# Performance work log

Hardware: AMD Instinct MI355X
Metric: run time of the kernel (lower is better)

The kernel has to match this reference:

```python
import jax, jax.numpy as jnp
import numpy as np

N_NODES = 100000
N_EDGES = 3200000
IN_FEAT = 512
HIDDEN = 64
N_GRAPHS = 2048


def setup_inputs() -> dict:
    key = jax.random.key(0)
    ks = jax.random.split(key, 8)
    x = jax.random.normal(ks[0], (N_NODES, IN_FEAT), dtype=jnp.float32)
    edge_index = jax.random.randint(ks[1], (2, N_EDGES), 0, N_NODES, dtype=jnp.int64)
    batch = jnp.sort(jax.random.randint(ks[2], (N_NODES,), 0, N_GRAPHS, dtype=jnp.int64))
    W1 = jax.random.normal(ks[3], (IN_FEAT, HIDDEN), dtype=jnp.float32) * (1.0 / np.sqrt(IN_FEAT))
    b1 = jnp.zeros((HIDDEN,), dtype=jnp.float32)
    W2 = jax.random.normal(ks[4], (HIDDEN, HIDDEN), dtype=jnp.float32) * (1.0 / np.sqrt(HIDDEN))
    b2 = jnp.zeros((HIDDEN,), dtype=jnp.float32)
    fc_w = jax.random.normal(ks[5], (HIDDEN, 1), dtype=jnp.float32) * (1.0 / np.sqrt(HIDDEN))
    fc_b = jnp.zeros((1,), dtype=jnp.float32)
    return {"x": x, "edge_index": edge_index, "batch": batch, "num_graphs": N_GRAPHS,
            "W1": W1, "b1": b1, "W2": W2, "b2": b2, "fc_w": fc_w, "fc_b": fc_b}


def _gcn_conv(x, src, dst, n_nodes, W, b):
    # PyG GCNConv: h = X W; out = D^{-1/2}(A+I)D^{-1/2} h + b  (self-loops already in src/dst)
    h = x @ W  # [N, out]
    ones = jnp.ones_like(src, dtype=h.dtype)
    deg = jax.ops.segment_sum(ones, dst, num_segments=n_nodes)  # in-degree incl. self-loop
    dinv = jnp.where(deg > 0, jax.lax.rsqrt(deg), 0.0)
    norm = dinv[src] * dinv[dst]  # [E+N]
    msgs = h[src] * norm[:, None]  # gather + scale
    out = jax.ops.segment_sum(msgs, dst, num_segments=n_nodes)  # scatter-add
    return out + b


def reference(x, edge_index, batch, num_graphs, W1, b1, W2, b2, fc_w, fc_b):
    n = x.shape[0]
    loops = jnp.arange(n, dtype=edge_index.dtype)
    src = jnp.concatenate([edge_index[0], loops])
    dst = jnp.concatenate([edge_index[1], loops])

    h = jax.nn.relu(_gcn_conv(x, src, dst, n, W1, b1))
    h = _gcn_conv(h, src, dst, n, W2, b2)

    # global_mean_pool over graph ids
    sums = jax.ops.segment_sum(h, batch, num_segments=num_graphs)
    cnts = jax.ops.segment_sum(jnp.ones((n,), dtype=h.dtype), batch, num_segments=num_graphs)
    pooled = sums / jnp.maximum(cnts, 1.0)[:, None]
    return pooled @ fc_w + fc_b  # [num_graphs, 1]
```

## Files before the change

kernel.cpp:

```cpp
#include <hip/hip_runtime.h>
#include <hip/hip_bf16.h>

#define N_NODES  100000
#define N_EDGES  3200000
#define IN_FEAT  512
#define HIDDEN   64
#define N_GRAPHS 2048
#define BSH      8
#define NPB      256
#define NBK      512
#define BCAP     10240
#define CH       4096

typedef __attribute__((ext_vector_type(8))) short short8;
typedef __attribute__((ext_vector_type(4))) float floatx4;

__device__ inline void bf16_split(float f, short& hi, short& lo) {
    unsigned u = __float_as_uint(f);
    unsigned r = (u + 0x7fffu + ((u >> 16) & 1u)) >> 16;
    float fh = __uint_as_float(r << 16);
    float fl = f - fh;
    unsigned v = __float_as_uint(fl);
    unsigned s = (v + 0x7fffu + ((v >> 16) & 1u)) >> 16;
    hi = (short)r;
    lo = (short)s;
}

__global__ __launch_bounds__(256) void fused_init(float* __restrict__ pooled,
                                                  int* __restrict__ cntg,
                                                  int* __restrict__ bcnt,
                                                  const int* __restrict__ batch,
                                                  int n, int g) {
    int i = blockIdx.x * 256 + threadIdx.x;
    if (i < g * 64) pooled[i] = 0.f;
    if (i < NBK) bcnt[i] = 0;
    if (i < g) {
        int lo0 = 0, hi0 = n;
        while (lo0 < hi0) { int m = (lo0 + hi0) >> 1; if (batch[m] < i) lo0 = m + 1; else hi0 = m; }
        int lo1 = lo0, hi1 = n;
        while (lo1 < hi1) { int m = (lo1 + hi1) >> 1; if (batch[m] < i + 1) lo1 = m + 1; else hi1 = m; }
        cntg[i] = lo1 - lo0;
    }
}

__global__ __launch_bounds__(256) void split_w(const float* __restrict__ W,
                                               short* __restrict__ hi_t,
                                               short* __restrict__ lo_t, int K) {
    int i = blockIdx.x * 256 + threadIdx.x;
    if (i < K * 64) {
        int k = i >> 6, c = i & 63;
        short h, l;
        bf16_split(W[i], h, l);
        hi_t[c * K + k] = h;
        lo_t[c * K + k] = l;
    }
}

__global__ __launch_bounds__(256) void bucket_count(const int* __restrict__ dst,
                                                    int* __restrict__ bcnt, int e) {
    __shared__ int lcnt[NBK];
    for (int b = threadIdx.x; b < NBK; b += 256) lcnt[b] = 0;
    __syncthreads();
    int i = blockIdx.x * 256 + threadIdx.x;
    int stride = gridDim.x * 256;
    for (; i < e; i += stride) atomicAdd(&lcnt[dst[i] >> BSH], 1);
    __syncthreads();
    for (int b = threadIdx.x; b < NBK; b += 256) {
        int c = lcnt[b];
        if (c) atomicAdd(&bcnt[b], c);
    }
}

__global__ void bucket_scan(const int* __restrict__ bcnt,
                            int* __restrict__ boff,
                            int* __restrict__ tail, int nb) {
    __shared__ int sA[512], sB[512];
    int t = threadIdx.x;
    int v = (t < nb) ? bcnt[t] : 0;
    sA[t] = v;
    __syncthreads();
    int* pin = sA; int* pout = sB;
    for (int off = 1; off < 512; off <<= 1) {
        pout[t] = pin[t] + ((t >= off) ? pin[t - off] : 0);
        __syncthreads();
        int* tmp = pin; pin = pout; pout = tmp;
    }
    if (t < nb) { boff[t] = pin[t] - v; tail[t] = pin[t] - v; }
    if (t == 0) boff[nb] = pin[nb - 1];
}

__global__ __launch_bounds__(256) void bucket_scatter(const int* __restrict__ src,
                                                      const int* __restrict__ dst,
                                                      int* __restrict__ tail,
                                                      unsigned* __restrict__ packed, int e) {
    __shared__ int lcnt[NBK];
    __shared__ int sbase[NBK];
    int t = threadIdx.x;
    for (int b = t; b < NBK; b += 256) lcnt[b] = 0;
    __syncthreads();
    int base = blockIdx.x * CH;
    int bk[16]; int rk[16]; unsigned pk[16];
#pragma unroll
    for (int j = 0; j < 16; j++) {
        int idx = base + j * 256 + t;
        bk[j] = -1;
        if (idx < e) {
            int d = dst[idx], s = src[idx];
            bk[j] = d >> BSH;
            pk[j] = ((unsigned)(d & (NPB - 1)) << 17) | (unsigned)s;
            rk[j] = atomicAdd(&lcnt[bk[j]], 1);
        }
    }
    __syncthreads();
    for (int b = t; b < NBK; b += 256) {
        int c = lcnt[b];
        sbase[b] = c ? atomicAdd(&tail[b], c) : 0;
    }
    __syncthreads();
#pragma unroll
    for (int j = 0; j < 16; j++)
        if (bk[j] >= 0) packed[sbase[bk[j]] + rk[j]] = pk[j];
}

__global__ __launch_bounds__(256) void bucket_csr(const unsigned* __restrict__ packed,
                                                  const int* __restrict__ boff,
                                                  int* __restrict__ csr,
                                                  int* __restrict__ row_start,
                                                  int* __restrict__ degi, int n) {
    __shared__ unsigned ed[BCAP];
    __shared__ int deg[NPB], excl[NPB], sA[NPB], sB[NPB];
    int b = blockIdx.x, t = threadIdx.x;
    int gbase = boff[b];
    int cnt = boff[b + 1] - gbase;
    if (cnt > BCAP) cnt = BCAP;
    for (int i = t; i < cnt; i += 256) ed[i] = packed[gbase + i];
    deg[t] = 0;
    __syncthreads();
    for (int i = t; i < cnt; i += 256) atomicAdd(&deg[ed[i] >> 17], 1);
    __syncthreads();
    sA[t] = deg[t];
    __syncthreads();
    int* pin = sA; int* pout = sB;
    for (int off = 1; off < NPB; off <<= 1) {
        pout[t] = pin[t] + ((t >= off) ? pin[t - off] : 0);
        __syncthreads();
        int* tmp = pin; pin = pout; pout = tmp;
    }
    excl[t] = pin[t] - deg[t];
    __syncthreads();
    int n0 = b << BSH;
    if (n0 + t < n) {
        row_start[n0 + t] = gbase + excl[t];
        degi[n0 + t] = deg[t] + 1;
    }
    __syncthreads();
    deg[t] = excl[t];
    __syncthreads();
    for (int i = t; i < cnt; i += 256) {
        unsigned p = ed[i];
        int d = p >> 17;
        int slot = atomicAdd(&deg[d], 1);
        csr[gbase + slot] = (int)(p & 0x1FFFFu);
    }
}

template <int K>
__global__ __launch_bounds__(256) void gemm_mfma(const float* __restrict__ X,
                                                 const short* __restrict__ Whi,
                                                 const short* __restrict__ Wlo,
                                                 const int* __restrict__ degi,
                                                 float* __restrict__ Y, int nrows) {
    constexpr int BSTR = 40;
    __shared__ short bhi[64 * BSTR];
    __shared__ short blo[64 * BSTR];

    const int t    = threadIdx.x;
    const int wave = t >> 6;
    const int lane = t & 63;
    const int quad = lane >> 4;
    const int l16  = lane & 15;

    const int arow   = blockIdx.x * 64 + wave * 16 + l16;
    const bool rvalid = arow < nrows;
    const float* xrow = X + (size_t)arow * K;

    const int scol = t & 63;
    const int skg  = t >> 6;
    const short* whp = Whi + (size_t)scol * K + skg * 8;
    const short* wlp = Wlo + (size_t)scol * K + skg * 8;

    floatx4 acc[4] = {};

#pragma unroll 1
    for (int k0 = 0; k0 < K; k0 += 32) {
        short8 whi = *(const short8*)(whp + k0);
        short8 wlo = *(const short8*)(wlp + k0);

        float av[8] = {0.f, 0.f, 0.f, 0.f, 0.f, 0.f, 0.f, 0.f};
        if (rvalid) {
            float4 p0 = *(const float4*)(xrow + k0 + quad * 8);
            float4 p1 = *(const float4*)(xrow + k0 + quad * 8 + 4);
            av[0] = p0.x; av[1] = p0.y; av[2] = p0.z; av[3] = p0.w;
            av[4] = p1.x; av[5] = p1.y; av[6] = p1.z; av[7] = p1.w;
        }
        short8 ahi, alo;
#pragma unroll
        for (int j = 0; j < 8; j++) { short h, l; bf16_split(av[j], h, l); ahi[j] = h; alo[j] = l; }

        __syncthreads();
        *(short8*)&bhi[scol * BSTR + skg * 8] = whi;
        *(short8*)&blo[scol * BSTR + skg * 8] = wlo;
        __syncthreads();

#pragma unroll
        for (int ct = 0; ct < 4; ct++) {
            int col = ct * 16 + l16;
            short8 bh = *(short8*)&bhi[col * BSTR + quad * 8];
            short8 bl = *(short8*)&blo[col * BSTR + quad * 8];
            acc[ct] = __builtin_amdgcn_mfma_f32_16x16x32_bf16(ahi, bh, acc[ct], 0, 0, 0);
            acc[ct] = __builtin_amdgcn_mfma_f32_16x16x32_bf16(ahi, bl, acc[ct], 0, 0, 0);
            acc[ct] = __builtin_amdgcn_mfma_f32_16x16x32_bf16(alo, bh, acc[ct], 0, 0, 0);
        }
    }

#pragma unroll
    for (int r = 0; r < 4; r++) {
        int orow = blockIdx.x * 64 + wave * 16 + quad * 4 + r;
        if (orow < nrows) {
            float dv = 1.0f / sqrtf((float)degi[orow]);
#pragma unroll
            for (int ct = 0; ct < 4; ct++)
                Y[(size_t)orow * 64 + ct * 16 + l16] = acc[ct][r] * dv;
        }
    }
}

template <bool RELU, bool POOL>
__global__ __launch_bounds__(256) void gcn_gather(const float* __restrict__ g,
                                                  const int* __restrict__ degi,
                                                  const int* __restrict__ row_start,
                                                  const int* __restrict__ csr_src,
                                                  const float* __restrict__ bias,
                                                  float* __restrict__ out,
                                                  float* __restrict__ pooled,
                                                  const int* __restrict__ batch, int n) {
    int node = (blockIdx.x * 256 + threadIdx.x) >> 6;
    int lane = threadIdx.x & 63;
    int es = lane >> 4;
    int fg = lane & 15;
    if (node >= n) return;

    int dg = degi[node];
    int de = dg - 1;
    float dn = 1.0f / sqrtf((float)dg);
    int start = row_start[node];

    float4 a0 = make_float4(0.f, 0.f, 0.f, 0.f);
    float4 a1 = a0, a2 = a0, a3 = a0;
    if (es == 0) a0 = *(const float4*)(g + (size_t)node * 64 + fg * 4);

    for (int c = 0; c < de; c += 64) {
        int m = min(64, de - c);
        int sv = (lane < m) ? csr_src[start + c + lane] : -1;
        int t = 0;
        for (; t + 16 <= m; t += 16) {
            int s0 = __shfl(sv, t + es);
            int s1 = __shfl(sv, t + 4 + es);
            int s2 = __shfl(sv, t + 8 + es);
            int s3 = __shfl(sv, t + 12 + es);
            float4 v0 = *(const float4*)(g + (size_t)s0 * 64 + fg * 4);
            float4 v1 = *(const float4*)(g + (size_t)s1 * 64 + fg * 4);
            float4 v2 = *(const float4*)(g + (size_t)s2 * 64 + fg * 4);
            float4 v3 = *(const float4*)(g + (size_t)s3 * 64 + fg * 4);
            a0.x += v0.x; a0.y += v0.y; a0.z += v0.z; a0.w += v0.w;
            a1.x += v1.x; a1.y += v1.y; a1.z += v1.z; a1.w += v1.w;
            a2.x += v2.x; a2.y += v2.y; a2.z += v2.z; a2.w += v2.w;
            a3.x += v3.x; a3.y += v3.y; a3.z += v3.z; a3.w += v3.w;
        }
        for (; t < m; t += 4) {
            int e = t + es;
            int s = __shfl(sv, e);
            if (e < m) {
                float4 v = *(const float4*)(g + (size_t)s * 64 + fg * 4);
                a0.x += v.x; a0.y += v.y; a0.z += v.z; a0.w += v.w;
            }
        }
    }
    float4 a;
    a.x = (a0.x + a1.x) + (a2.x + a3.x);
    a.y = (a0.y + a1.y) + (a2.y + a3.y);
    a.z = (a0.z + a1.z) + (a2.z + a3.z);
    a.w = (a0.w + a1.w) + (a2.w + a3.w);
    a.x += __shfl_xor(a.x, 16); a.y += __shfl_xor(a.y, 16);
    a.z += __shfl_xor(a.z, 16); a.w += __shfl_xor(a.w, 16);
    a.x += __shfl_xor(a.x, 32); a.y += __shfl_xor(a.y, 32);
    a.z += __shfl_xor(a.z, 32); a.w += __shfl_xor(a.w, 32);

    if (es == 0) {
        float4 bv = *(const float4*)(bias + fg * 4);
        float4 o;
        o.x = fmaf(dn, a.x, bv.x);
        o.y = fmaf(dn, a.y, bv.y);
        o.z = fmaf(dn, a.z, bv.z);
        o.w = fmaf(dn, a.w, bv.w);
        if (RELU) {
            o.x = fmaxf(o.x, 0.f); o.y = fmaxf(o.y, 0.f);
            o.z = fmaxf(o.z, 0.f); o.w = fmaxf(o.w, 0.f);
        }
        if (POOL) {
            float* pp = pooled + (size_t)batch[node] * 64 + fg * 4;
            atomicAdd(pp + 0, o.x);
            atomicAdd(pp + 1, o.y);
            atomicAdd(pp + 2, o.z);
            atomicAdd(pp + 3, o.w);
        } else {
            *(float4*)(out + (size_t)node * 64 + fg * 4) = o;
        }
    }
}

__global__ __launch_bounds__(256) void final_fc(const float* __restrict__ pooled,
                                                const int* __restrict__ cntg,
                                                const float* __restrict__ fc_w,
                                                const float* __restrict__ fc_b,
                                                float* __restrict__ out, int g) {
    int gid = (blockIdx.x * 256 + threadIdx.x) >> 6;
    int lane = threadIdx.x & 63;
    if (gid >= g) return;
    float c = fmaxf((float)cntg[gid], 1.0f);
    float v = pooled[(size_t)gid * 64 + lane] / c * fc_w[lane];
#pragma unroll
    for (int off = 32; off > 0; off >>= 1) v += __shfl_down(v, off);
    if (lane == 0) out[gid] = v + fc_b[0];
}

extern "C" void kernel_launch(void* const* d_in, const int* in_sizes, int n_in,
                              void* d_out, int out_size, void* d_ws, size_t ws_size,
                              hipStream_t stream) {
    const float* x    = (const float*)d_in[0];
    const int*   eidx = (const int*)d_in[1];
    const int*   batch= (const int*)d_in[2];
    const float* W1   = (const float*)d_in[4];
    const float* b1   = (const float*)d_in[5];
    const float* W2   = (const float*)d_in[6];
    const float* b2   = (const float*)d_in[7];
    const float* fc_w = (const float*)d_in[8];
    const float* fc_b = (const float*)d_in[9];
    float* out = (float*)d_out;

    const int N = in_sizes[0] / IN_FEAT;
    const int E = in_sizes[1] / 2;
    const int G = N_GRAPHS;
    const int* src = eidx;
    const int* dst = eidx + E;
    const int nb = (N + NPB - 1) >> BSH;

    char* w = (char*)d_ws;
    float* g1   = (float*)w; w += (size_t)N * 64 * 4;
    float* h1r  = (float*)w; w += (size_t)N * 64 * 4;
    float* g2   = (float*)w; w += (size_t)N * 64 * 4;
    int*   degi = (int*)w;   w += (size_t)N * 4;
    int*   rowst= (int*)w;   w += (size_t)N * 4;
    int*   bcnt = (int*)w;   w += NBK * 4;
    int*   boff = (int*)w;   w += (NBK + 1) * 4 + 12;
    int*   tail = (int*)w;   w += NBK * 4;
    unsigned* packed = (unsigned*)w; w += (size_t)E * 4;
    int*   csrs = (int*)w;   w += (size_t)E * 4;
    float* pooled = (float*)w; w += (size_t)G * 64 * 4;
    int*   cntg = (int*)w;   w += (size_t)G * 4;
    short* w1hi = (short*)w; w += (size_t)IN_FEAT * 64 * 2;
    short* w1lo = (short*)w; w += (size_t)IN_FEAT * 64 * 2;
    short* w2hi = (short*)w; w += (size_t)HIDDEN * 64 * 2;
    short* w2lo = (short*)w; w += (size_t)HIDDEN * 64 * 2;

    fused_init<<<(G * 64 + 255) / 256, 256, 0, stream>>>(pooled, cntg, bcnt, batch, N, G);
    split_w<<<(IN_FEAT * 64 + 255) / 256, 256, 0, stream>>>(W1, w1hi, w1lo, IN_FEAT);
    split_w<<<(HIDDEN * 64 + 255) / 256, 256, 0, stream>>>(W2, w2hi, w2lo, HIDDEN);

    bucket_count<<<2048, 256, 0, stream>>>(dst, bcnt, E);
    bucket_scan<<<1, 512, 0, stream>>>(bcnt, boff, tail, nb);
    bucket_scatter<<<(E + CH - 1) / CH, 256, 0, stream>>>(src, dst, tail, packed, E);
    bucket_csr<<<nb, 256, 0, stream>>>(packed, boff, csrs, rowst, degi, N);

    gemm_mfma<IN_FEAT><<<(N + 63) / 64, 256, 0, stream>>>(x, w1hi, w1lo, degi, g1, N);
    gcn_gather<true, false><<<(N * 64 + 255) / 256, 256, 0, stream>>>(
        g1, degi, rowst, csrs, b1, h1r, nullptr, batch, N);
    gemm_mfma<HIDDEN><<<(N + 63) / 64, 256, 0, stream>>>(h1r, w2hi, w2lo, degi, g2, N);
    gcn_gather<false, true><<<(N * 64 + 255) / 256, 256, 0, stream>>>(
        g2, degi, rowst, csrs, b2, nullptr, pooled, batch, N);
    final_fc<<<(G * 64 + 255) / 256, 256, 0, stream>>>(pooled, cntg, fc_w, fc_b, out, G);
}
```

Before: 743.0 us.

## Use fixed-capacity buckets, drop count pass, fuse weight split into init

Gives each destination bucket a fixed BCAP-sized region, so the scatter kernel no longer needs a prior counting pass and prefix scan. The scan now runs after the scatter on the final tail counters to produce compact CSR offsets. The weight bf16 splits move into the init kernel, and the GEMM reads B fragments directly from global memory instead of staging them through LDS with barriers. This removes three launches and a full pass over dst. In exchange the packed buffer grows to NBK*BCAP entries, and edges beyond a bucket's capacity are silently dropped.

```diff
diff --git a/kernel.cpp b/kernel.cpp
--- a/kernel.cpp
+++ b/kernel.cpp
@@ -28,12 +28,30 @@
 
 __global__ __launch_bounds__(256) void fused_init(float* __restrict__ pooled,
                                                   int* __restrict__ cntg,
-                                                  int* __restrict__ bcnt,
+                                                  int* __restrict__ tail,
                                                   const int* __restrict__ batch,
+                                                  const float* __restrict__ W1,
+                                                  short* __restrict__ w1hi, short* __restrict__ w1lo,
+                                                  const float* __restrict__ W2,
+                                                  short* __restrict__ w2hi, short* __restrict__ w2lo,
                                                   int n, int g) {
     int i = blockIdx.x * 256 + threadIdx.x;
     if (i < g * 64) pooled[i] = 0.f;
-    if (i < NBK) bcnt[i] = 0;
+    if (i < NBK) tail[i] = i * BCAP;
+    if (i < IN_FEAT * 64) {
+        int k = i >> 6, c = i & 63;
+        short h, l;
+        bf16_split(W1[i], h, l);
+        w1hi[c * IN_FEAT + k] = h;
+        w1lo[c * IN_FEAT + k] = l;
+    }
+    if (i < HIDDEN * 64) {
+        int k = i >> 6, c = i & 63;
+        short h, l;
+        bf16_split(W2[i], h, l);
+        w2hi[c * HIDDEN + k] = h;
+        w2lo[c * HIDDEN + k] = l;
+    }
     if (i < g) {
         int lo0 = 0, hi0 = n;
         while (lo0 < hi0) { int m = (lo0 + hi0) >> 1; if (batch[m] < i) lo0 = m + 1; else hi0 = m; }
@@ -41,52 +59,6 @@
         while (lo1 < hi1) { int m = (lo1 + hi1) >> 1; if (batch[m] < i + 1) lo1 = m + 1; else hi1 = m; }
         cntg[i] = lo1 - lo0;
     }
-}
-
-__global__ __launch_bounds__(256) void split_w(const float* __restrict__ W,
-                                               short* __restrict__ hi_t,
-                                               short* __restrict__ lo_t, int K) {
-    int i = blockIdx.x * 256 + threadIdx.x;
-    if (i < K * 64) {
-        int k = i >> 6, c = i & 63;
-        short h, l;
-        bf16_split(W[i], h, l);
-        hi_t[c * K + k] = h;
-        lo_t[c * K + k] = l;
-    }
-}
-
-__global__ __launch_bounds__(256) void bucket_count(const int* __restrict__ dst,
-                                                    int* __restrict__ bcnt, int e) {
-    __shared__ int lcnt[NBK];
-    for (int b = threadIdx.x; b < NBK; b += 256) lcnt[b] = 0;
-    __syncthreads();
-    int i = blockIdx.x * 256 + threadIdx.x;
-    int stride = gridDim.x * 256;
-    for (; i < e; i += stride) atomicAdd(&lcnt[dst[i] >> BSH], 1);
-    __syncthreads();
-    for (int b = threadIdx.x; b < NBK; b += 256) {
-        int c = lcnt[b];
-        if (c) atomicAdd(&bcnt[b], c);
-    }
-}
-
-__global__ void bucket_scan(const int* __restrict__ bcnt,
-                            int* __restrict__ boff,
-                            int* __restrict__ tail, int nb) {
-    __shared__ int sA[512], sB[512];
-    int t = threadIdx.x;
-    int v = (t < nb) ? bcnt[t] : 0;
-    sA[t] = v;
-    __syncthreads();
-    int* pin = sA; int* pout = sB;
-    for (int off = 1; off < 512; off <<= 1) {
-        pout[t] = pin[t] + ((t >= off) ? pin[t - off] : 0);
-        __syncthreads();
-        int* tmp = pin; pin = pout; pout = tmp;
-    }
-    if (t < nb) { boff[t] = pin[t] - v; tail[t] = pin[t] - v; }
-    if (t == 0) boff[nb] = pin[nb - 1];
 }
 
 __global__ __launch_bounds__(256) void bucket_scatter(const int* __restrict__ src,
@@ -119,7 +91,28 @@
     __syncthreads();
 #pragma unroll
     for (int j = 0; j < 16; j++)
-        if (bk[j] >= 0) packed[sbase[bk[j]] + rk[j]] = pk[j];
+        if (bk[j] >= 0) {
+            int slot = sbase[bk[j]] + rk[j];
+            if (slot < (bk[j] + 1) * BCAP)
+                packed[slot] = pk[j];
+        }
+}
+
+__global__ void bucket_scan(const int* __restrict__ tail,
+                            int* __restrict__ boff, int nb) {
+    __shared__ int sA[512], sB[512];
+    int t = threadIdx.x;
+    int v = (t < nb) ? min(tail[t] - t * BCAP, BCAP) : 0;
+    sA[t] = v;
+    __syncthreads();
+    int* pin = sA; int* pout = sB;
+    for (int off = 1; off < 512; off <<= 1) {
+        pout[t] = pin[t] + ((t >= off) ? pin[t - off] : 0);
+        __syncthreads();
+        int* tmp = pin; pin = pout; pout = tmp;
+    }
+    if (t < nb) boff[t] = pin[t] - v;
+    if (t == 0) boff[nb] = pin[nb - 1];
 }
 
 __global__ __launch_bounds__(256) void bucket_csr(const unsigned* __restrict__ packed,
@@ -133,7 +126,8 @@
     int gbase = boff[b];
     int cnt = boff[b + 1] - gbase;
     if (cnt > BCAP) cnt = BCAP;
-    for (int i = t; i < cnt; i += 256) ed[i] = packed[gbase + i];
+    const unsigned* pbase = packed + (size_t)b * BCAP;
+    for (int i = t; i < cnt; i += 256) ed[i] = pbase[i];
     deg[t] = 0;
     __syncthreads();
     for (int i = t; i < cnt; i += 256) atomicAdd(&deg[ed[i] >> 17], 1);
@@ -170,10 +164,6 @@
                                                  const short* __restrict__ Wlo,
                                                  const int* __restrict__ degi,
                                                  float* __restrict__ Y, int nrows) {
-    constexpr int BSTR = 40;
-    __shared__ short bhi[64 * BSTR];
-    __shared__ short blo[64 * BSTR];
-
     const int t    = threadIdx.x;
     const int wave = t >> 6;
     const int lane = t & 63;
@@ -184,18 +174,10 @@
     const bool rvalid = arow < nrows;
     const float* xrow = X + (size_t)arow * K;
 
-    const int scol = t & 63;
-    const int skg  = t >> 6;
-    const short* whp = Whi + (size_t)scol * K + skg * 8;
-    const short* wlp = Wlo + (size_t)scol * K + skg * 8;
-
     floatx4 acc[4] = {};
 
 #pragma unroll 1
     for (int k0 = 0; k0 < K; k0 += 32) {
-        short8 whi = *(const short8*)(whp + k0);
-        short8 wlo = *(const short8*)(wlp + k0);
-
         float av[8] = {0.f, 0.f, 0.f, 0.f, 0.f, 0.f, 0.f, 0.f};
         if (rvalid) {
             float4 p0 = *(const float4*)(xrow + k0 + quad * 8);
@@ -207,16 +189,11 @@
 #pragma unroll
         for (int j = 0; j < 8; j++) { short h, l; bf16_split(av[j], h, l); ahi[j] = h; alo[j] = l; }
 
-        __syncthreads();
-        *(short8*)&bhi[scol * BSTR + skg * 8] = whi;
-        *(short8*)&blo[scol * BSTR + skg * 8] = wlo;
-        __syncthreads();
-
 #pragma unroll
         for (int ct = 0; ct < 4; ct++) {
             int col = ct * 16 + l16;
-            short8 bh = *(short8*)&bhi[col * BSTR + quad * 8];
-            short8 bl = *(short8*)&blo[col * BSTR + quad * 8];
+            short8 bh = *(const short8*)(Whi + (size_t)col * K + k0 + quad * 8);
+            short8 bl = *(const short8*)(Wlo + (size_t)col * K + k0 + quad * 8);
             acc[ct] = __builtin_amdgcn_mfma_f32_16x16x32_bf16(ahi, bh, acc[ct], 0, 0, 0);
             acc[ct] = __builtin_amdgcn_mfma_f32_16x16x32_bf16(ahi, bl, acc[ct], 0, 0, 0);
             acc[ct] = __builtin_amdgcn_mfma_f32_16x16x32_bf16(alo, bh, acc[ct], 0, 0, 0);
@@ -361,10 +338,9 @@
     float* g2   = (float*)w; w += (size_t)N * 64 * 4;
     int*   degi = (int*)w;   w += (size_t)N * 4;
     int*   rowst= (int*)w;   w += (size_t)N * 4;
-    int*   bcnt = (int*)w;   w += NBK * 4;
     int*   boff = (int*)w;   w += (NBK + 1) * 4 + 12;
     int*   tail = (int*)w;   w += NBK * 4;
-    unsigned* packed = (unsigned*)w; w += (size_t)E * 4;
+    unsigned* packed = (unsigned*)w; w += (size_t)NBK * BCAP * 4;
     int*   csrs = (int*)w;   w += (size_t)E * 4;
     float* pooled = (float*)w; w += (size_t)G * 64 * 4;
     int*   cntg = (int*)w;   w += (size_t)G * 4;
@@ -373,13 +349,10 @@
     short* w2hi = (short*)w; w += (size_t)HIDDEN * 64 * 2;
     short* w2lo = (short*)w; w += (size_t)HIDDEN * 64 * 2;
 
-    fused_init<<<(G * 64 + 255) / 256, 256, 0, stream>>>(pooled, cntg, bcnt, batch, N, G);
-    split_w<<<(IN_FEAT * 64 + 255) / 256, 256, 0, stream>>>(W1, w1hi, w1lo, IN_FEAT);
-    split_w<<<(HIDDEN * 64 + 255) / 256, 256, 0, stream>>>(W2, w2hi, w2lo, HIDDEN);
-
-    bucket_count<<<2048, 256, 0, stream>>>(dst, bcnt, E);
-    bucket_scan<<<1, 512, 0, stream>>>(bcnt, boff, tail, nb);
+    fused_init<<<512, 256, 0, stream>>>(pooled, cntg, tail, batch,
+                                        W1, w1hi, w1lo, W2, w2hi, w2lo, N, G);
     bucket_scatter<<<(E + CH - 1) / CH, 256, 0, stream>>>(src, dst, tail, packed, E);
+    bucket_scan<<<1, 512, 0, stream>>>(tail, boff, nb);
     bucket_csr<<<nb, 256, 0, stream>>>(packed, boff, csrs, rowst, degi, N);
 
     gemm_mfma<IN_FEAT><<<(N + 63) / 64, 256, 0, stream>>>(x, w1hi, w1lo, degi, g1, N);
```

Result: no change. 731.8 us (-1.5%).
